# Optimization experiments

Hardware: AMD Instinct MI355X
Metric: run time of the kernel (lower is better)

The kernel has to match this reference:

```python
import jax, jax.numpy as jnp
import numpy as np

B, S, D, H, E = 2, 2048, 1024, 4096, 8


def setup_inputs() -> dict:
    key = jax.random.key(0)
    k0, k1, k2, k3 = jax.random.split(key, 4)
    x = jax.random.normal(k0, (B, S, D), dtype=jnp.float32)
    router_w = jax.random.normal(k1, (E, D), dtype=jnp.float32) * 0.02   # Top2Router Linear weight [E, D]
    w1 = jax.random.normal(k2, (E, D, H), dtype=jnp.float32) * 0.02      # stacked fc1 weights (transposed: x @ w1[e])
    w2 = jax.random.normal(k3, (E, H, D), dtype=jnp.float32) * 0.02      # stacked fc2 weights
    return {"x": x, "router_w": router_w, "w1": w1, "w2": w2}


def reference(x, router_w, w1, w2):
    # x: [B, S, D] -> flatten tokens. Single-rank EP: all-to-all is identity,
    # microbatch split is a pure overlap trick, per-token math unchanged.
    b, s, d = x.shape
    e = router_w.shape[0]
    xf = x.reshape(-1, d)                                     # [T, D]
    # Top-2 router with renormalized gate weights
    probs = jax.nn.softmax(xf @ router_w.T, axis=-1)          # [T, E]
    topv, topi = jax.lax.top_k(probs, 2)                      # [T, 2]
    topv = topv / (topv.sum(axis=-1, keepdims=True) + 1e-9)
    # Combine weights per expert: cw[t,e] = sum_k topv[t,k] * [topi[t,k]==e]
    cw = (jax.nn.one_hot(topi, e, dtype=xf.dtype) * topv[..., None]).sum(axis=1)  # [T, E]
    # Expert MLPs (dense-over-experts reference for the grouped GEMM)
    h = jax.nn.gelu(jnp.einsum('td,edh->teh', xf, w1), approximate=False)  # [T, E, H]
    y = jnp.einsum('teh,ehd->ted', h, w2)                                   # [T, E, D]
    out = jnp.einsum('te,ted->td', cw, y)                                   # weighted combine (scatter-add equiv.)
    return out.reshape(b, s, d)
```

## Files before the change

### kernel.cpp

```cpp
#include <hip/hip_runtime.h>

#define T_TOK 4096
#define DIM   1024
#define HID   4096
#define NEXP  8
#define MAXROWS 9216

typedef unsigned short u16;
typedef __attribute__((ext_vector_type(8))) short short8;
typedef __attribute__((ext_vector_type(4))) float f32x4;
typedef __attribute__((ext_vector_type(4))) unsigned short u16x4;
typedef __attribute__((ext_vector_type(8))) unsigned short u16x8;

typedef __attribute__((address_space(3))) unsigned int lds_uint;
typedef const __attribute__((address_space(1))) unsigned int gbl_uint;

__device__ __forceinline__ u16 f2bf(float f) {
    union { float f; unsigned int u; } v; v.f = f;
    unsigned int r = v.u + 0x7fffu + ((v.u >> 16) & 1u);
    return (u16)(r >> 16);
}

__device__ __forceinline__ float gelu_f(float v) {
    float u = 1.5957691216f * (v + 0.044715f * v * v * v);
    float s = 1.0f / (1.0f + __expf(-u));
    return v * s;
}

__global__ __launch_bounds__(256)
void transpose_blocked(const float* __restrict__ w1, u16* __restrict__ w1t,
                       const float* __restrict__ w2, u16* __restrict__ w2t,
                       int* __restrict__ counts) {
    int b = blockIdx.x;
    if (b == 0 && threadIdx.x < NEXP) counts[threadIdx.x] = 0;
    const float* in; u16* out; int C, KT, ct, kt, e;
    if (b < 4096) {
        e = b >> 9; int t = b & 511; ct = t & 31; kt = t >> 5;
        in = w1; out = w1t; C = HID; KT = 16;
    } else {
        b -= 4096;
        e = b >> 9; int t = b & 511; ct = t & 7; kt = t >> 3;
        in = w2; out = w2t; C = DIM; KT = 64;
    }
    __shared__ u16 tl[64 * 130];
    size_t mo = (size_t)e * DIM * HID;
    const float* ip = in + mo + (size_t)(kt * 64) * C + ct * 128;
    u16* op = out + mo + (size_t)(ct * KT + kt) * 8192;
    int tid = threadIdx.x;
#pragma unroll
    for (int j = 0; j < 8; ++j) {
        int id = tid + 256 * j;
        int kr = id >> 5, cg = id & 31;
        f32x4 v = *(const f32x4*)(ip + (size_t)kr * C + 4 * cg);
        u16x4 w; w.x = f2bf(v.x); w.y = f2bf(v.y); w.z = f2bf(v.z); w.w = f2bf(v.w);
        *(u16x4*)(tl + kr * 130 + 4 * cg) = w;
    }
    __syncthreads();
#pragma unroll
    for (int j = 0; j < 4; ++j) {
        int id = tid + 256 * j;
        int n = id >> 3, c = id & 7;
        u16x8 o;
#pragma unroll
        for (int m = 0; m < 8; ++m) o[m] = tl[(c * 8 + m) * 130 + n];
        *(u16x8*)(op + id * 8) = o;
    }
}

__global__ __launch_bounds__(256)
void router_k(const float* __restrict__ x, const float* __restrict__ rw,
              int* __restrict__ counts, int* __restrict__ tE,
              int* __restrict__ tS, float* __restrict__ tG) {
    int wave = threadIdx.x >> 6, lane = threadIdx.x & 63;
    int t = blockIdx.x * 4 + wave;
    const float* xr = x + (size_t)t * DIM;
    float xv[16];
#pragma unroll
    for (int i = 0; i < 16; ++i) xv[i] = xr[lane + 64*i];
    float lg[NEXP];
#pragma unroll
    for (int e = 0; e < NEXP; ++e) {
        const float* wr_ = rw + e * DIM;
        float a = 0.f;
#pragma unroll
        for (int i = 0; i < 16; ++i) a += xv[i] * wr_[lane + 64*i];
        lg[e] = a;
    }
#pragma unroll
    for (int off = 32; off > 0; off >>= 1)
#pragma unroll
        for (int e = 0; e < NEXP; ++e) lg[e] += __shfl_xor(lg[e], off, 64);
    if (lane == 0) {
        float mx = lg[0];
        for (int e = 1; e < NEXP; ++e) mx = fmaxf(mx, lg[e]);
        float p[NEXP], s = 0.f;
        for (int e = 0; e < NEXP; ++e) { p[e] = expf(lg[e] - mx); s += p[e]; }
        float inv_s = 1.f / s;
        for (int e = 0; e < NEXP; ++e) p[e] *= inv_s;
        int i0 = 0;
        for (int e = 1; e < NEXP; ++e) if (p[e] > p[i0]) i0 = e;
        int i1 = (i0 == 0) ? 1 : 0;
        for (int e = 0; e < NEXP; ++e) if (e != i0 && p[e] > p[i1]) i1 = e;
        float v0 = p[i0], v1 = p[i1];
        float inv = 1.f / (v0 + v1 + 1e-9f);
        int s0 = atomicAdd(&counts[i0], 1);
        int s1 = atomicAdd(&counts[i1], 1);
        tE[2*t] = i0;  tE[2*t+1] = i1;
        tS[2*t] = s0;  tS[2*t+1] = s1;
        tG[2*t] = v0 * inv;  tG[2*t+1] = v1 * inv;
    }
}

__device__ __forceinline__ int pbase_of(const int* __restrict__ counts, int e) {
    int pb = 0;
#pragma unroll
    for (int i = 0; i < NEXP; ++i) {
        int pad = ((counts[i] + 127) >> 7) << 7;
        pb += (i < e) ? pad : 0;
    }
    return pb;
}

__global__ __launch_bounds__(256)
void gather_k(const float* __restrict__ x, const int* __restrict__ tE,
              const int* __restrict__ tS, const int* __restrict__ counts,
              u16* __restrict__ xg) {
    int a = blockIdx.x;
    int t = a >> 1, k = a & 1;
    int e = tE[2*t + k];
    int row = pbase_of(counts, e) + tS[2*t + k];
    const f32x4* xr = (const f32x4*)(x + (size_t)t * DIM);
    u16x4* o = (u16x4*)(xg + (size_t)row * DIM);
    int i = threadIdx.x;
    f32x4 v = xr[i];
    u16x4 r; r.x = f2bf(v.x); r.y = f2bf(v.y); r.z = f2bf(v.z); r.w = f2bf(v.w);
    o[i] = r;
}

template<int K, int KSPLIT, int NX, bool GELU, typename OutT>
__global__ __launch_bounds__(256)
void gemm_bt(const u16* __restrict__ A, const u16* __restrict__ BtAll,
             OutT* __restrict__ C, const int* __restrict__ counts,
             int N, size_t cstride) {
    int lin = blockIdx.x;
    int e = lin & 7;
    int kk = lin >> 3;
    int ct = kk % NX;
    int rest = kk / NX;
    int ks = rest % KSPLIT;
    int mt = rest / KSPLIT;
    int cnt = counts[e];
    if (mt * 128 >= cnt) return;
    int row0 = pbase_of(counts, e) + mt * 128;
    const u16* Bt = BtAll + (size_t)e * N * K;
    OutT* Cp = C + (size_t)ks * cstride;
    int col0 = ct * 128;
    const int kb0 = ks * (K / KSPLIT);
    constexpr int KT = K / 64;
    constexpr int KITER = K / KSPLIT / 64;

    __shared__ __align__(16) u16 smem[128 * 128];
    u16* As = smem;
    u16* Bs = smem + 128 * 64;

    int tid = threadIdx.x;
    int lane = tid & 63;
    int w = tid >> 6;
    int quad = lane >> 4, m16 = lane & 15;
    int wr = (w >> 1) * 64, wc = (w & 1) * 64;
    int rsub = lane >> 3;
    int kch  = lane & 7;
    int kchs = kch ^ rsub;

    const u16* ga[4];
    const u16* gb[4];
#pragma unroll
    for (int i = 0; i < 4; ++i) {
        int r = (w * 4 + i) * 8 + rsub;
        ga[i] = A  + (size_t)(row0 + r) * K + kb0 + kchs * 8;
        gb[i] = Bt + ((size_t)ct * KT + kb0 / 64) * 8192 + r * 64 + kchs * 8;
    }
    int sw = m16 & 7;
    const u16* aP0 = As + (wr + m16) * 64 + ((quad       ^ sw) << 3);
    const u16* aP1 = As + (wr + m16) * 64 + (((4 + quad) ^ sw) << 3);
    const u16* bP0 = Bs + (wc + m16) * 64 + ((quad       ^ sw) << 3);
    const u16* bP1 = Bs + (wc + m16) * 64 + (((4 + quad) ^ sw) << 3);

    f32x4 acc[4][4] = {};

    for (int kit = 0; kit < KITER; ++kit) {
#pragma unroll
        for (int i = 0; i < 4; ++i) {
            int grp = w * 4 + i;
            __builtin_amdgcn_global_load_lds((gbl_uint*)ga[i], (lds_uint*)(As + grp * 512), 16, 0, 0);
            __builtin_amdgcn_global_load_lds((gbl_uint*)gb[i], (lds_uint*)(Bs + grp * 512), 16, 0, 0);
            ga[i] += 64; gb[i] += 8192;
        }
        __syncthreads();
        {
            short8 af[4], bfr[4];
#pragma unroll
            for (int mi = 0; mi < 4; ++mi) af[mi]  = *(const short8*)(aP0 + mi * 1024);
#pragma unroll
            for (int ni = 0; ni < 4; ++ni) bfr[ni] = *(const short8*)(bP0 + ni * 1024);
#pragma unroll
            for (int mi = 0; mi < 4; ++mi)
#pragma unroll
                for (int ni = 0; ni < 4; ++ni)
                    acc[mi][ni] = __builtin_amdgcn_mfma_f32_16x16x32_bf16(af[mi], bfr[ni], acc[mi][ni], 0, 0, 0);
#pragma unroll
            for (int mi = 0; mi < 4; ++mi) af[mi]  = *(const short8*)(aP1 + mi * 1024);
#pragma unroll
            for (int ni = 0; ni < 4; ++ni) bfr[ni] = *(const short8*)(bP1 + ni * 1024);
#pragma unroll
            for (int mi = 0; mi < 4; ++mi)
#pragma unroll
                for (int ni = 0; ni < 4; ++ni)
                    acc[mi][ni] = __builtin_amdgcn_mfma_f32_16x16x32_bf16(af[mi], bfr[ni], acc[mi][ni], 0, 0, 0);
        }
        __syncthreads();
    }

    if (GELU) {
#pragma unroll
        for (int mi = 0; mi < 4; ++mi) {
#pragma unroll
            for (int r = 0; r < 4; ++r) {
                int row = wr + mi * 16 + quad * 4 + r;
#pragma unroll
                for (int ni = 0; ni < 4; ++ni) {
                    int col = wc + ni * 16 + m16;
                    int c16 = col >> 3, w8 = col & 7;
                    smem[row * 128 + (((c16 ^ (row & 15)) << 3) | w8)] = f2bf(gelu_f(acc[mi][ni][r]));
                }
            }
        }
        __syncthreads();
        int row_b = tid >> 4, c16_b = tid & 15;
        const u16* ls = smem + row_b * 128 + (((c16_b ^ (row_b & 15)) << 3));
        u16* gp = (u16*)Cp + (size_t)(row0 + row_b) * N + col0 + c16_b * 8;
#pragma unroll
        for (int j = 0; j < 8; ++j) {
            *(u16x8*)gp = *(const u16x8*)ls;
            ls += 16 * 128;
            gp += (size_t)16 * N;
        }
    } else {
        float* gp = (float*)Cp + (size_t)(row0 + wr + quad * 4) * N + col0 + wc + m16;
#pragma unroll
        for (int mi = 0; mi < 4; ++mi)
#pragma unroll
            for (int r = 0; r < 4; ++r) {
                float* rp = gp + (size_t)(mi * 16 + r) * N;
#pragma unroll
                for (int ni = 0; ni < 4; ++ni)
                    rp[ni * 16] = acc[mi][ni][r];
            }
    }
}

__global__ __launch_bounds__(256)
void combine_k(const float* __restrict__ p0, const float* __restrict__ p1,
               const int* __restrict__ tE, const int* __restrict__ tS,
               const float* __restrict__ tG, const int* __restrict__ counts,
               float* __restrict__ out) {
    int t = blockIdx.x;
    int e0 = tE[2*t], e1 = tE[2*t+1];
    int r0 = pbase_of(counts, e0) + tS[2*t];
    int r1 = pbase_of(counts, e1) + tS[2*t+1];
    float g0 = tG[2*t], g1 = tG[2*t+1];
    int i = threadIdx.x;
    f32x4 a0 = ((const f32x4*)(p0 + (size_t)r0 * DIM))[i];
    f32x4 b0 = ((const f32x4*)(p1 + (size_t)r0 * DIM))[i];
    f32x4 a1 = ((const f32x4*)(p0 + (size_t)r1 * DIM))[i];
    f32x4 b1 = ((const f32x4*)(p1 + (size_t)r1 * DIM))[i];
    f32x4* o = (f32x4*)(out + (size_t)t * DIM);
    o[i] = g0 * (a0 + b0) + g1 * (a1 + b1);
}

extern "C" void kernel_launch(void* const* d_in, const int* in_sizes, int n_in,
                              void* d_out, int out_size, void* d_ws, size_t ws_size,
                              hipStream_t stream) {
    const float* x  = (const float*)d_in[0];
    const float* rw = (const float*)d_in[1];
    const float* w1 = (const float*)d_in[2];
    const float* w2 = (const float*)d_in[3];
    float* out = (float*)d_out;

    char* ws = (char*)d_ws;
    u16* w1t = (u16*)(ws + 0);
    u16* xg  = (u16*)(ws + 67108864ull);
    u16* w2t = (u16*)(ws + 85983232ull);
    u16* hb  = (u16*)(ws + 153092096ull);
    float* p0 = (float*)(ws + 0);
    float* p1 = (float*)(ws + 37748736ull);
    int* ctrl   = (int*)(ws + 228589568ull);
    int* counts = ctrl;
    int* tE     = ctrl + 32;
    int* tS     = ctrl + 32 + 8192;
    float* tG   = (float*)(ctrl + 32 + 16384);

    transpose_blocked<<<8192, 256, 0, stream>>>(w1, w1t, w2, w2t, counts);
    router_k<<<T_TOK / 4, 256, 0, stream>>>(x, rw, counts, tE, tS, tG);
    gather_k<<<T_TOK * 2, 256, 0, stream>>>(x, tE, tS, counts, xg);
    gemm_bt<DIM, 1, 32, true, u16><<<2560, 256, 0, stream>>>(
        xg, w1t, hb, counts, HID, 0);
    gemm_bt<HID, 2, 8, false, float><<<1280, 256, 0, stream>>>(
        hb, w2t, p0, counts, DIM, (size_t)MAXROWS * DIM);
    combine_k<<<T_TOK, 256, 0, stream>>>(p0, p1, tE, tS, tG, counts, out);
}
```

Baseline: 645.4 us.

## Add 256x256-tile pipelined GEMM for fc1 and drop split-K in fc2

Adds a new 512-thread grouped GEMM with 256x256 output tiles, double-buffered LDS staging through global_load_lds, interleaved barriers and setprio around the MFMA bursts, and inline-asm ds_read_b128 fragment loads. It replaces the 128-tile fc1 GEMM with GELU epilogue. The fc2 GEMM drops its two-way K split, so combine reads a single partial buffer instead of summing two. The aim is more data reuse per tile, load latency hidden behind MFMA work, and no extra partial-sum traffic. In exchange, fc1 launches fewer, larger blocks, which can leave the device underfilled when expert counts are ragged, and fc2 now has half as many blocks.

```diff
diff --git a/kernel.cpp b/kernel.cpp
--- a/kernel.cpp
+++ b/kernel.cpp
@@ -13,6 +13,7 @@
 typedef __attribute__((ext_vector_type(8))) unsigned short u16x8;
 
 typedef __attribute__((address_space(3))) unsigned int lds_uint;
+typedef __attribute__((address_space(3))) u16 lds_u16;
 typedef const __attribute__((address_space(1))) unsigned int gbl_uint;
 
 __device__ __forceinline__ u16 f2bf(float f) {
@@ -25,6 +26,12 @@
     float u = 1.5957691216f * (v + 0.044715f * v * v * v);
     float s = 1.0f / (1.0f + __expf(-u));
     return v * s;
+}
+
+__device__ __forceinline__ short8 ds_read128(unsigned byte_addr) {
+    short8 r;
+    asm volatile("ds_read_b128 %0, %1" : "=v"(r) : "v"(byte_addr));
+    return r;
 }
 
 __global__ __launch_bounds__(256)
@@ -135,6 +142,175 @@
     f32x4 v = xr[i];
     u16x4 r; r.x = f2bf(v.x); r.y = f2bf(v.y); r.z = f2bf(v.z); r.w = f2bf(v.w);
     o[i] = r;
+}
+
+template<int K, bool GELU, typename OutT>
+__global__ __launch_bounds__(512, 2)
+void gemm256(const u16* __restrict__ A, const u16* __restrict__ BtAll,
+             OutT* __restrict__ C, const int* __restrict__ counts, int N) {
+    constexpr int NT = K / 64;
+    constexpr int KT = K / 64;
+    int lin = blockIdx.x;
+    int e = lin & 7, kk = lin >> 3;
+    int ctb = kk & 15, mt = kk >> 4;
+    int cnt = counts[e];
+    if (mt * 256 >= cnt) return;
+    int row0 = pbase_of(counts, e) + mt * 256;
+    int limit = cnt - mt * 256;
+    const u16* Bt = BtAll + (size_t)e * N * K;
+    int col0 = ctb * 256;
+
+    __shared__ __align__(16) u16 smem[65536];
+
+    int tid = threadIdx.x;
+    int lane = tid & 63, w = tid >> 6;
+    int quad = lane >> 4, m16 = lane & 15;
+    int wr = (w >> 2) * 128, wc = (w & 3) * 64;
+
+    const u16* gA[2]; const u16* gB[2]; int lds8[2];
+#pragma unroll
+    for (int l = 0; l < 2; ++l) {
+        int slot = tid + l * 512;
+        int r = slot >> 2, cs = slot & 3;
+        int gk = cs ^ ((r ^ (r >> 2)) & 3);
+        int ra = row0 + r; if (ra > MAXROWS - 1) ra = MAXROWS - 1;
+        gA[l] = A + (size_t)ra * K + gk * 8;
+        gB[l] = Bt + (size_t)((ctb * 2 + (r >> 7)) * KT) * 8192
+                   + (r & 127) * 64 + gk * 8;
+        lds8[l] = slot * 8;
+    }
+#define STG_A(l, t, s, buf) __builtin_amdgcn_global_load_lds( \
+    (gbl_uint*)(gA[l] + (t) * 64 + (s) * 32), \
+    (lds_uint*)(smem + (buf) * 32768 + (s) * 8192 + lds8[l]), 16, 0, 0)
+#define STG_B(l, t, s, buf) __builtin_amdgcn_global_load_lds( \
+    (gbl_uint*)(gB[l] + (t) * 8192 + (s) * 32), \
+    (lds_uint*)(smem + (buf) * 32768 + 16384 + (s) * 8192 + lds8[l]), 16, 0, 0)
+
+    int f3 = (m16 ^ (m16 >> 2)) & 3;
+    unsigned smb = (unsigned)(size_t)(lds_u16*)smem;
+    unsigned aF = smb + (unsigned)((wr + m16) * 64 + ((quad ^ f3) << 4));
+    unsigned bF = smb + 32768u + (unsigned)((wc + m16) * 64 + ((quad ^ f3) << 4));
+
+    f32x4 acc[8][4] = {};
+
+    STG_A(0, 0, 0, 0); STG_A(1, 0, 0, 0);
+    STG_B(0, 0, 0, 0); STG_B(1, 0, 0, 0);
+    STG_A(0, 0, 1, 0); STG_A(1, 0, 1, 0);
+    STG_B(0, 0, 1, 0); STG_B(1, 0, 1, 0);
+    asm volatile("s_waitcnt vmcnt(4)" ::: "memory");
+    __builtin_amdgcn_s_barrier();
+
+    short8 af[8], bf[2], bg[2];
+    for (int t = 0; t < NT; ++t) {
+        unsigned db = (t & 1) ? 65536u : 0u;
+        int nb = (t + 1) & 1;
+        bool st = (t + 1 < NT);
+#pragma unroll
+        for (int mi = 0; mi < 8; ++mi) af[mi] = ds_read128(aF + db + mi * 1024);
+        bf[0] = ds_read128(bF + db);
+        bf[1] = ds_read128(bF + db + 1024);
+        if (st) { STG_A(0, t + 1, 0, nb); STG_A(1, t + 1, 0, nb); }
+        __builtin_amdgcn_s_barrier();
+        asm volatile("s_waitcnt lgkmcnt(0)" ::: "memory");
+        __builtin_amdgcn_sched_barrier(0);
+        __builtin_amdgcn_s_setprio(1);
+#pragma unroll
+        for (int mi = 0; mi < 8; ++mi) {
+            acc[mi][0] = __builtin_amdgcn_mfma_f32_16x16x32_bf16(af[mi], bf[0], acc[mi][0], 0, 0, 0);
+            acc[mi][1] = __builtin_amdgcn_mfma_f32_16x16x32_bf16(af[mi], bf[1], acc[mi][1], 0, 0, 0);
+        }
+        __builtin_amdgcn_s_setprio(0);
+        __builtin_amdgcn_s_barrier();
+        bg[0] = ds_read128(bF + db + 2048);
+        bg[1] = ds_read128(bF + db + 3072);
+        if (st) { STG_B(0, t + 1, 0, nb); STG_B(1, t + 1, 0, nb); }
+        __builtin_amdgcn_s_barrier();
+        asm volatile("s_waitcnt lgkmcnt(0)" ::: "memory");
+        __builtin_amdgcn_sched_barrier(0);
+        __builtin_amdgcn_s_setprio(1);
+#pragma unroll
+        for (int mi = 0; mi < 8; ++mi) {
+            acc[mi][2] = __builtin_amdgcn_mfma_f32_16x16x32_bf16(af[mi], bg[0], acc[mi][2], 0, 0, 0);
+            acc[mi][3] = __builtin_amdgcn_mfma_f32_16x16x32_bf16(af[mi], bg[1], acc[mi][3], 0, 0, 0);
+        }
+        __builtin_amdgcn_s_setprio(0);
+        if (st) asm volatile("s_waitcnt vmcnt(4)" ::: "memory");
+        else    asm volatile("s_waitcnt vmcnt(0)" ::: "memory");
+        __builtin_amdgcn_s_barrier();
+#pragma unroll
+        for (int mi = 0; mi < 8; ++mi) af[mi] = ds_read128(aF + db + 16384 + mi * 1024);
+        bf[0] = ds_read128(bF + db + 16384);
+        bf[1] = ds_read128(bF + db + 16384 + 1024);
+        if (st) { STG_A(0, t + 1, 1, nb); STG_A(1, t + 1, 1, nb); }
+        __builtin_amdgcn_s_barrier();
+        asm volatile("s_waitcnt lgkmcnt(0)" ::: "memory");
+        __builtin_amdgcn_sched_barrier(0);
+        __builtin_amdgcn_s_setprio(1);
+#pragma unroll
+        for (int mi = 0; mi < 8; ++mi) {
+            acc[mi][0] = __builtin_amdgcn_mfma_f32_16x16x32_bf16(af[mi], bf[0], acc[mi][0], 0, 0, 0);
+            acc[mi][1] = __builtin_amdgcn_mfma_f32_16x16x32_bf16(af[mi], bf[1], acc[mi][1], 0, 0, 0);
+        }
+        __builtin_amdgcn_s_setprio(0);
+        __builtin_amdgcn_s_barrier();
+        bg[0] = ds_read128(bF + db + 16384 + 2048);
+        bg[1] = ds_read128(bF + db + 16384 + 3072);
+        if (st) { STG_B(0, t + 1, 1, nb); STG_B(1, t + 1, 1, nb); }
+        __builtin_amdgcn_s_barrier();
+        asm volatile("s_waitcnt lgkmcnt(0)" ::: "memory");
+        __builtin_amdgcn_sched_barrier(0);
+        __builtin_amdgcn_s_setprio(1);
+#pragma unroll
+        for (int mi = 0; mi < 8; ++mi) {
+            acc[mi][2] = __builtin_amdgcn_mfma_f32_16x16x32_bf16(af[mi], bg[0], acc[mi][2], 0, 0, 0);
+            acc[mi][3] = __builtin_amdgcn_mfma_f32_16x16x32_bf16(af[mi], bg[1], acc[mi][3], 0, 0, 0);
+        }
+        __builtin_amdgcn_s_setprio(0);
+        if (st) asm volatile("s_waitcnt vmcnt(4)" ::: "memory");
+        __builtin_amdgcn_s_barrier();
+    }
+#undef STG_A
+#undef STG_B
+
+    if (GELU) {
+        __syncthreads();
+#pragma unroll
+        for (int mi = 0; mi < 8; ++mi) {
+#pragma unroll
+            for (int r = 0; r < 4; ++r) {
+                int row = wr + mi * 16 + quad * 4 + r;
+#pragma unroll
+                for (int ni = 0; ni < 4; ++ni) {
+                    int col = wc + ni * 16 + m16;
+                    int ch = col >> 3, w8 = col & 7;
+                    smem[row * 256 + (((ch ^ (row & 31)) << 3) | w8)] = f2bf(gelu_f(acc[mi][ni][r]));
+                }
+            }
+        }
+        __syncthreads();
+        int rr = tid >> 5, ch = tid & 31;
+#pragma unroll
+        for (int it = 0; it < 16; ++it) {
+            int row = it * 16 + rr;
+            if (row < limit) {
+                u16x8 v = *(const u16x8*)(smem + row * 256 + ((ch ^ (row & 31)) << 3));
+                *(u16x8*)((u16*)C + (size_t)(row0 + row) * N + col0 + ch * 8) = v;
+            }
+        }
+    } else {
+#pragma unroll
+        for (int mi = 0; mi < 8; ++mi)
+#pragma unroll
+            for (int r = 0; r < 4; ++r) {
+                int rl = wr + mi * 16 + quad * 4 + r;
+                if (rl < limit) {
+                    float* rp = (float*)C + (size_t)(row0 + rl) * N + col0 + wc + m16;
+#pragma unroll
+                    for (int ni = 0; ni < 4; ++ni)
+                        rp[ni * 16] = acc[mi][ni][r];
+                }
+            }
+    }
 }
 
 template<int K, int KSPLIT, int NX, bool GELU, typename OutT>
@@ -198,25 +374,25 @@
         }
         __syncthreads();
         {
-            short8 af[4], bfr[4];
-#pragma unroll
-            for (int mi = 0; mi < 4; ++mi) af[mi]  = *(const short8*)(aP0 + mi * 1024);
+            short8 af2[4], bfr[4];
+#pragma unroll
+            for (int mi = 0; mi < 4; ++mi) af2[mi] = *(const short8*)(aP0 + mi * 1024);
 #pragma unroll
             for (int ni = 0; ni < 4; ++ni) bfr[ni] = *(const short8*)(bP0 + ni * 1024);
 #pragma unroll
             for (int mi = 0; mi < 4; ++mi)
 #pragma unroll
                 for (int ni = 0; ni < 4; ++ni)
-                    acc[mi][ni] = __builtin_amdgcn_mfma_f32_16x16x32_bf16(af[mi], bfr[ni], acc[mi][ni], 0, 0, 0);
-#pragma unroll
-            for (int mi = 0; mi < 4; ++mi) af[mi]  = *(const short8*)(aP1 + mi * 1024);
+                    acc[mi][ni] = __builtin_amdgcn_mfma_f32_16x16x32_bf16(af2[mi], bfr[ni], acc[mi][ni], 0, 0, 0);
+#pragma unroll
+            for (int mi = 0; mi < 4; ++mi) af2[mi] = *(const short8*)(aP1 + mi * 1024);
 #pragma unroll
             for (int ni = 0; ni < 4; ++ni) bfr[ni] = *(const short8*)(bP1 + ni * 1024);
 #pragma unroll
             for (int mi = 0; mi < 4; ++mi)
 #pragma unroll
                 for (int ni = 0; ni < 4; ++ni)
-                    acc[mi][ni] = __builtin_amdgcn_mfma_f32_16x16x32_bf16(af[mi], bfr[ni], acc[mi][ni], 0, 0, 0);
+                    acc[mi][ni] = __builtin_amdgcn_mfma_f32_16x16x32_bf16(af2[mi], bfr[ni], acc[mi][ni], 0, 0, 0);
         }
         __syncthreads();
     }
@@ -260,7 +436,7 @@
 }
 
 __global__ __launch_bounds__(256)
-void combine_k(const float* __restrict__ p0, const float* __restrict__ p1,
+void combine_k(const float* __restrict__ p0,
                const int* __restrict__ tE, const int* __restrict__ tS,
                const float* __restrict__ tG, const int* __restrict__ counts,
                float* __restrict__ out) {
@@ -271,11 +447,9 @@
     float g0 = tG[2*t], g1 = tG[2*t+1];
     int i = threadIdx.x;
     f32x4 a0 = ((const f32x4*)(p0 + (size_t)r0 * DIM))[i];
-    f32x4 b0 = ((const f32x4*)(p1 + (size_t)r0 * DIM))[i];
     f32x4 a1 = ((const f32x4*)(p0 + (size_t)r1 * DIM))[i];
-    f32x4 b1 = ((const f32x4*)(p1 + (size_t)r1 * DIM))[i];
     f32x4* o = (f32x4*)(out + (size_t)t * DIM);
-    o[i] = g0 * (a0 + b0) + g1 * (a1 + b1);
+    o[i] = g0 * a0 + g1 * a1;
 }
 
 extern "C" void kernel_launch(void* const* d_in, const int* in_sizes, int n_in,
@@ -293,7 +467,6 @@
     u16* w2t = (u16*)(ws + 85983232ull);
     u16* hb  = (u16*)(ws + 153092096ull);
     float* p0 = (float*)(ws + 0);
-    float* p1 = (float*)(ws + 37748736ull);
     int* ctrl   = (int*)(ws + 228589568ull);
     int* counts = ctrl;
     int* tE     = ctrl + 32;
@@ -303,9 +476,8 @@
     transpose_blocked<<<8192, 256, 0, stream>>>(w1, w1t, w2, w2t, counts);
     router_k<<<T_TOK / 4, 256, 0, stream>>>(x, rw, counts, tE, tS, tG);
     gather_k<<<T_TOK * 2, 256, 0, stream>>>(x, tE, tS, counts, xg);
-    gemm_bt<DIM, 1, 32, true, u16><<<2560, 256, 0, stream>>>(
-        xg, w1t, hb, counts, HID, 0);
-    gemm_bt<HID, 2, 8, false, float><<<1280, 256, 0, stream>>>(
-        hb, w2t, p0, counts, DIM, (size_t)MAXROWS * DIM);
-    combine_k<<<T_TOK, 256, 0, stream>>>(p0, p1, tE, tS, tG, counts, out);
-}
+    gemm256<DIM, true, u16><<<640, 512, 0, stream>>>(xg, w1t, hb, counts, HID);
+    gemm_bt<HID, 1, 8, false, float><<<640, 256, 0, stream>>>(
+        hb, w2t, p0, counts, DIM, 0);
+    combine_k<<<T_TOK, 256, 0, stream>>>(p0, tE, tS, tG, counts, out);
+}
```

Measured after the change: 655.4 us. About the same (+1.6%).
